# Kernel tuning notes

Measured on AMD Instinct MI355X. Metric: run time of the kernel, lower is better.

Reference implementation:

```python
import jax, jax.numpy as jnp
import numpy as np

K = 3      # kernel size
PAD = 1    # kernel_size // 2


def _deform_conv(x, offset, w_def):
    """mmcv DeformConv (deform_groups=1, stride=1, dilation=1, no bias).
    x: [B,C,H,W], offset: [B,2*K*K,H,W] ordered (dy,dx) per kernel tap, w_def: [O,C,K,K].
    Bilinear sampling with zero padding outside the feature map.
    """
    B, C, H, W = x.shape
    kk = K * K
    off = offset.reshape(B, kk, 2, H, W)
    # kernel-tap grid (row-major: ky, kx)
    ar = jnp.arange(K)
    gy, gx = jnp.meshgrid(ar, ar, indexing='ij')
    gy = gy.reshape(kk)
    gx = gx.reshape(kk)
    hh = jnp.arange(H, dtype=x.dtype)
    ww = jnp.arange(W, dtype=x.dtype)
    # sampling positions: p0 - pad + kernel tap + learned offset  -> [B,kk,H,W]
    ys = hh[None, None, :, None] - PAD + gy[None, :, None, None] + off[:, :, 0]
    xs = ww[None, None, None, :] - PAD + gx[None, :, None, None] + off[:, :, 1]

    y0 = jnp.floor(ys)
    x0 = jnp.floor(xs)
    ly = ys - y0
    lx = xs - x0

    xf = x.reshape(B, C, H * W)

    def gather(yi, xi):
        valid = (yi >= 0) & (yi <= H - 1) & (xi >= 0) & (xi <= W - 1)
        yc = jnp.clip(yi, 0, H - 1).astype(jnp.int32)
        xc = jnp.clip(xi, 0, W - 1).astype(jnp.int32)
        idx = (yc * W + xc).reshape(B, 1, kk * H * W)
        g = jnp.take_along_axis(xf, idx, axis=2).reshape(B, C, kk, H, W)
        return g * valid.reshape(B, 1, kk, H, W).astype(x.dtype)

    # bilinear interpolation, per-corner zero masking == zero padding
    v = (gather(y0, x0) * ((1 - ly) * (1 - lx))[:, None]
         + gather(y0, x0 + 1) * ((1 - ly) * lx)[:, None]
         + gather(y0 + 1, x0) * (ly * (1 - lx))[:, None]
         + gather(y0 + 1, x0 + 1) * (ly * lx)[:, None])  # [B,C,kk,H,W]

    O = w_def.shape[0]
    return jnp.einsum('bckhw,ock->bohw', v, w_def.reshape(O, C, kk))


def setup_inputs() -> dict:
    key = jax.random.key(0)
    k1, k2, k3, k4 = jax.random.split(key, 4)
    B, C_in, C_off, C_out, H, W = 4, 128, 64, 128, 128, 128
    x = jax.random.normal(k1, (B, C_in, H, W), dtype=jnp.float32)
    off = jax.random.normal(k2, (B, C_off, H, W), dtype=jnp.float32)
    # NOTE: the torch module zero-inits the offset conv; we use small random
    # weights so the deformable gather path is actually exercised.
    w_off = 0.1 * jax.random.normal(k3, (2 * K * K, C_off), dtype=jnp.float32)
    b_off = jnp.zeros((2 * K * K,), dtype=jnp.float32)
    w_def = jax.random.normal(k4, (C_out, C_in, K, K), dtype=jnp.float32) / np.sqrt(C_in * K * K)
    return {"x": x, "off": off, "w_off": w_off, "b_off": b_off, "w_def": w_def}


def reference(x, off, w_off, b_off, w_def):
    # 1x1 offset conv
    offset = jnp.einsum('oc,bchw->bohw', w_off, off) + b_off[None, :, None, None]
    # deformable conv + ReLU
    return jax.nn.relu(_deform_conv(x, offset, w_def))
```

## Files before the change

### kernel.cpp

```cpp
#include <hip/hip_runtime.h>
#include <stdint.h>

typedef __attribute__((ext_vector_type(8))) short short8;
typedef __attribute__((ext_vector_type(4))) float f32x4;

constexpr int Hc = 128, Wc = 128, HWc = Hc * Wc;
constexpr int Cin = 128, Cout = 128;
constexpr int OffC = 18, OffIn = 64;

__device__ __forceinline__ float bf2f(unsigned short u) {
    return __builtin_bit_cast(float, (unsigned)u << 16);
}
__device__ __forceinline__ unsigned short f2bf(float f) {
    unsigned u = __builtin_bit_cast(unsigned, f);
    return (unsigned short)((u + 0x7FFFu + ((u >> 16) & 1u)) >> 16);
}

__global__ void k_offconv(const float* __restrict__ off, const float* __restrict__ w_off,
                          const float* __restrict__ b_off, float* __restrict__ offset) {
    __shared__ float wsm[OffC * OffIn];
    __shared__ float bsm[OffC];
    int tid = threadIdx.x;
    for (int i = tid; i < OffC * OffIn; i += 256) wsm[i] = w_off[i];
    if (tid < OffC) bsm[tid] = b_off[tid];
    __syncthreads();
    int g = blockIdx.x * 256 + tid;
    int b = g >> 14, hw = g & (HWc - 1);
    const float* offb = off + b * OffIn * HWc + hw;
    float acc[OffC];
#pragma unroll
    for (int o = 0; o < OffC; ++o) acc[o] = bsm[o];
    for (int c = 0; c < OffIn; ++c) {
        float v = offb[c << 14];
#pragma unroll
        for (int o = 0; o < OffC; ++o) acc[o] += wsm[o * OffIn + c] * v;
    }
    float* outb = offset + b * OffC * HWc + hw;
#pragma unroll
    for (int o = 0; o < OffC; ++o) outb[o << 14] = acc[o];
}

__global__ void k_xpose(const float* __restrict__ x, unsigned short* __restrict__ xt) {
    __shared__ float tile[128][65];
    int blk = blockIdx.x;
    int b = blk >> 8;
    int hw0 = (blk & 255) << 6;
    const float* xb = x + b * Cin * HWc;
    int tid = threadIdx.x;
#pragma unroll
    for (int k = 0; k < 32; ++k) {
        int e = tid + k * 256;
        int c = e >> 6, p = e & 63;
        tile[c][p] = xb[(c << 14) + hw0 + p];
    }
    __syncthreads();
    unsigned short* xtb = xt + ((b << 14) + hw0) * Cin;
#pragma unroll
    for (int k = 0; k < 16; ++k) {
        int e = (tid + k * 256) * 2;
        int p = e >> 7, c = e & 127;
        unsigned lo = f2bf(tile[c][p]);
        unsigned hi = f2bf(tile[c + 1][p]);
        *(unsigned*)(xtb + e) = lo | (hi << 16);
    }
}

__global__ void k_wprep(const float* __restrict__ wd, unsigned short* __restrict__ wt) {
    int i = blockIdx.x * 256 + threadIdx.x;
    int kk = i >> 14, o = (i >> 7) & 127, c = i & 127;
    wt[i] = f2bf(wd[((o << 7) + c) * 9 + kk]);
}

__global__ __launch_bounds__(512, 4)
void k_deform(const unsigned short* __restrict__ xt, const float* __restrict__ offset,
              const unsigned short* __restrict__ wt, float* __restrict__ out) {
    __shared__ float offs[OffC][128];
    __shared__ __align__(16) unsigned short vt[2][128 * 128];

    int tid = threadIdx.x;
    int bid = blockIdx.x;
    int swz = (bid & 7) * 64 + (bid >> 3);
    int b = swz >> 7;
    int hw0 = (swz & 127) << 7;

    const float* offg = offset + b * OffC * HWc + hw0;
    for (int i = tid; i < OffC * 128; i += 512)
        offs[i >> 7][i & 127] = offg[((i >> 7) << 14) + (i & 127)];
    __syncthreads();

    int px = tid >> 2;
    int cq = tid & 3;
    int c0 = cq * 8;
    int h = (hw0 + px) >> 7, w = (hw0 + px) & 127;
    const unsigned short* xb = xt + (size_t)(b << 14) * Cin;
    char* vtb = (char*)vt;

    float cw[4]; int cb[4];
    auto calc_params = [&](int tap) {
        float dy = offs[2 * tap][px], dx = offs[2 * tap + 1][px];
        float ys = (float)(h - 1 + tap / 3) + dy;
        float xs = (float)(w - 1 + tap % 3) + dx;
        float y0f = floorf(ys), x0f = floorf(xs);
        float ly = ys - y0f, lx = xs - x0f;
        int y0 = (int)y0f, x0 = (int)x0f;
#pragma unroll
        for (int cr = 0; cr < 4; ++cr) {
            int yi = y0 + (cr >> 1), xi = x0 + (cr & 1);
            bool valid = (yi >= 0) && (yi < Hc) && (xi >= 0) && (xi < Wc);
            float wy = (cr >> 1) ? ly : 1.0f - ly;
            float wx = (cr & 1) ? lx : 1.0f - lx;
            int yc = yi < 0 ? 0 : (yi > Hc - 1 ? Hc - 1 : yi);
            int xc = xi < 0 ? 0 : (xi > Wc - 1 ? Wc - 1 : xi);
            cw[cr] = valid ? wy * wx : 0.0f;
            cb[cr] = ((yc << 7) + xc) << 7;
        }
    };
    auto issue = [&](short8* r, int i) {
#pragma unroll
        for (int cr = 0; cr < 4; ++cr)
            r[cr] = *(const short8*)(xb + cb[cr] + c0 + i * 32);
    };
    auto consume = [&](short8* r, int i, int buf) {
        float v[8];
#pragma unroll
        for (int k = 0; k < 8; ++k) {
            v[k] = cw[0] * bf2f((unsigned short)r[0][k])
                 + cw[1] * bf2f((unsigned short)r[1][k])
                 + cw[2] * bf2f((unsigned short)r[2][k])
                 + cw[3] * bf2f((unsigned short)r[3][k]);
        }
        short8 pk;
#pragma unroll
        for (int k = 0; k < 8; ++k) pk[k] = (short)f2bf(v[k]);
        int byteoff = ((px << 8) + ((c0 + i * 32) << 1)) ^ ((px & 7) << 4);
        *(short8*)(vtb + buf * 32768 + byteoff) = pk;
    };

    int lane = tid & 63, wave = tid >> 6;
    int obase = (wave >> 2) << 6;
    int pbase = (wave & 3) << 5;

    f32x4 acc[4][2];
#pragma unroll
    for (int i = 0; i < 4; ++i)
#pragma unroll
        for (int j = 0; j < 2; ++j)
            acc[i][j] = (f32x4){0.f, 0.f, 0.f, 0.f};

    auto mfma_half = [&](int buf, int tap, int kb0) {
        const unsigned short* wtap = wt + (tap << 14);
#pragma unroll
        for (int kb = kb0; kb < kb0 + 2; ++kb) {
            int kc = (kb << 5) + ((lane >> 4) << 3);
            int p0 = pbase + (lane & 15);
            int p1 = p0 + 16;
            short8 b0 = *(const short8*)(vtb + buf * 32768 + ((((p0 << 8) + (kc << 1)) ^ ((p0 & 7) << 4))));
            short8 b1 = *(const short8*)(vtb + buf * 32768 + ((((p1 << 8) + (kc << 1)) ^ ((p1 & 7) << 4))));
            short8 aa[4];
#pragma unroll
            for (int ot = 0; ot < 4; ++ot)
                aa[ot] = *(const short8*)(wtap + (obase + (ot << 4) + (lane & 15)) * 128 + kc);
#pragma unroll
            for (int ot = 0; ot < 4; ++ot) {
                acc[ot][0] = __builtin_amdgcn_mfma_f32_16x16x32_bf16(aa[ot], b0, acc[ot][0], 0, 0, 0);
                acc[ot][1] = __builtin_amdgcn_mfma_f32_16x16x32_bf16(aa[ot], b1, acc[ot][1], 0, 0, 0);
            }
        }
    };

    short8 r0[4], r1[4];

    calc_params(0);
    issue(r0, 0); issue(r1, 1);
    consume(r0, 0, 0); issue(r0, 2);
    consume(r1, 1, 0); issue(r1, 3);
    consume(r0, 2, 0); consume(r1, 3, 0);
    __syncthreads();

    for (int t = 0; t < 9; ++t) {
        int cur = t & 1;
        if (t < 8) {
            calc_params(t + 1);
            issue(r0, 0); issue(r1, 1);
        }
        mfma_half(cur, t, 0);
        if (t < 8) {
            consume(r0, 0, cur ^ 1); issue(r0, 2);
            consume(r1, 1, cur ^ 1); issue(r1, 3);
        }
        mfma_half(cur, t, 2);
        if (t < 8) {
            consume(r0, 2, cur ^ 1); consume(r1, 3, cur ^ 1);
        }
        __syncthreads();
    }

    float* outb = out + (size_t)(b * Cout) * HWc + hw0;
#pragma unroll
    for (int ot = 0; ot < 4; ++ot)
#pragma unroll
        for (int pb = 0; pb < 2; ++pb)
#pragma unroll
            for (int j = 0; j < 4; ++j) {
                int o = obase + (ot << 4) + ((lane >> 4) << 2) + j;
                int p = pbase + (pb << 4) + (lane & 15);
                float v = acc[ot][pb][j];
                outb[(o << 14) + p] = v > 0.f ? v : 0.f;
            }
}

extern "C" void kernel_launch(void* const* d_in, const int* in_sizes, int n_in,
                              void* d_out, int out_size, void* d_ws, size_t ws_size,
                              hipStream_t stream) {
    const float* x     = (const float*)d_in[0];
    const float* off   = (const float*)d_in[1];
    const float* w_off = (const float*)d_in[2];
    const float* b_off = (const float*)d_in[3];
    const float* w_def = (const float*)d_in[4];
    float* out = (float*)d_out;

    char* ws = (char*)d_ws;
    float* offset      = (float*)ws;
    unsigned short* xt = (unsigned short*)(ws + 4718592);
    unsigned short* wt = (unsigned short*)(ws + 4718592 + 16777216);

    hipLaunchKernelGGL(k_offconv, dim3(256),  dim3(256), 0, stream, off, w_off, b_off, offset);
    hipLaunchKernelGGL(k_xpose,   dim3(1024), dim3(256), 0, stream, x, xt);
    hipLaunchKernelGGL(k_wprep,   dim3(576),  dim3(256), 0, stream, w_def, wt);
    hipLaunchKernelGGL(k_deform,  dim3(512),  dim3(512), 0, stream, xt, offset, wt, out);
}
```

Measured before the change: 206.7 us.

## Gather bilinear samples directly into MFMA B-fragments, dropping LDS staging

The deform kernel no longer stages the offsets and blended samples in shared memory with double buffering and barriers. Each wave now loads its own offsets, gathers the four bilinear corners straight into the register layout the MFMA B operand expects, and blends them in registers. Each wave now covers all 128 output channels for 32 pixels, with 256-thread blocks instead of 512. This removes LDS traffic and __syncthreads, but each block reads every weight fragment four times from global/L2 and holds more accumulator registers, and gather latency is no longer overlapped with compute.

```diff
diff --git a/kernel.cpp b/kernel.cpp
--- a/kernel.cpp
+++ b/kernel.cpp
@@ -71,33 +71,33 @@
     wt[i] = f2bf(wd[((o << 7) + c) * 9 + kk]);
 }
 
-__global__ __launch_bounds__(512, 4)
+__global__ __launch_bounds__(256)
 void k_deform(const unsigned short* __restrict__ xt, const float* __restrict__ offset,
               const unsigned short* __restrict__ wt, float* __restrict__ out) {
-    __shared__ float offs[OffC][128];
-    __shared__ __align__(16) unsigned short vt[2][128 * 128];
-
     int tid = threadIdx.x;
+    int lane = tid & 63, wave = tid >> 6;
     int bid = blockIdx.x;
     int swz = (bid & 7) * 64 + (bid >> 3);
     int b = swz >> 7;
     int hw0 = (swz & 127) << 7;
+    int p0 = hw0 + (wave << 5) + (lane & 15);
+    int p1 = p0 + 16;
+    int cg = lane >> 4;
 
-    const float* offg = offset + b * OffC * HWc + hw0;
-    for (int i = tid; i < OffC * 128; i += 512)
-        offs[i >> 7][i & 127] = offg[((i >> 7) << 14) + (i & 127)];
-    __syncthreads();
+    const unsigned short* xb = xt + ((size_t)b << 21);
+    const float* offp = offset + (size_t)b * (OffC * HWc);
 
-    int px = tid >> 2;
-    int cq = tid & 3;
-    int c0 = cq * 8;
-    int h = (hw0 + px) >> 7, w = (hw0 + px) & 127;
-    const unsigned short* xb = xt + (size_t)(b << 14) * Cin;
-    char* vtb = (char*)vt;
+    int h0 = p0 >> 7, w0 = p0 & 127;
+    int h1 = p1 >> 7, w1 = p1 & 127;
 
-    float cw[4]; int cb[4];
-    auto calc_params = [&](int tap) {
-        float dy = offs[2 * tap][px], dx = offs[2 * tap + 1][px];
+    f32x4 acc[8][2];
+#pragma unroll
+    for (int i = 0; i < 8; ++i)
+#pragma unroll
+        for (int j = 0; j < 2; ++j)
+            acc[i][j] = (f32x4){0.f, 0.f, 0.f, 0.f};
+
+    auto cparm = [&](int tap, float dy, float dx, int h, int w, float* cw, int* cb) {
         float ys = (float)(h - 1 + tap / 3) + dy;
         float xs = (float)(w - 1 + tap % 3) + dx;
         float y0f = floorf(ys), x0f = floorf(xs);
@@ -115,97 +115,65 @@
             cb[cr] = ((yc << 7) + xc) << 7;
         }
     };
-    auto issue = [&](short8* r, int i) {
-#pragma unroll
-        for (int cr = 0; cr < 4; ++cr)
-            r[cr] = *(const short8*)(xb + cb[cr] + c0 + i * 32);
-    };
-    auto consume = [&](short8* r, int i, int buf) {
-        float v[8];
-#pragma unroll
-        for (int k = 0; k < 8; ++k) {
-            v[k] = cw[0] * bf2f((unsigned short)r[0][k])
-                 + cw[1] * bf2f((unsigned short)r[1][k])
-                 + cw[2] * bf2f((unsigned short)r[2][k])
-                 + cw[3] * bf2f((unsigned short)r[3][k]);
-        }
+
+    auto blend = [&](const short8* r, const float* cw) -> short8 {
         short8 pk;
 #pragma unroll
-        for (int k = 0; k < 8; ++k) pk[k] = (short)f2bf(v[k]);
-        int byteoff = ((px << 8) + ((c0 + i * 32) << 1)) ^ ((px & 7) << 4);
-        *(short8*)(vtb + buf * 32768 + byteoff) = pk;
+        for (int j = 0; j < 8; ++j) {
+            float v = cw[0] * bf2f((unsigned short)r[0][j])
+                    + cw[1] * bf2f((unsigned short)r[1][j])
+                    + cw[2] * bf2f((unsigned short)r[2][j])
+                    + cw[3] * bf2f((unsigned short)r[3][j]);
+            pk[j] = (short)f2bf(v);
+        }
+        return pk;
     };
 
-    int lane = tid & 63, wave = tid >> 6;
-    int obase = (wave >> 2) << 6;
-    int pbase = (wave & 3) << 5;
+    float cw0[4], cw1[4]; int cb0[4], cb1[4];
+    float dy0 = offp[p0], dx0 = offp[(1 << 14) + p0];
+    float dy1 = offp[p1], dx1 = offp[(1 << 14) + p1];
 
-    f32x4 acc[4][2];
+    for (int t = 0; t < 9; ++t) {
+        cparm(t, dy0, dx0, h0, w0, cw0, cb0);
+        cparm(t, dy1, dx1, h1, w1, cw1, cb1);
+        if (t < 8) {
+            dy0 = offp[((2 * t + 2) << 14) + p0]; dx0 = offp[((2 * t + 3) << 14) + p0];
+            dy1 = offp[((2 * t + 2) << 14) + p1]; dx1 = offp[((2 * t + 3) << 14) + p1];
+        }
+        const unsigned short* wtap = wt + (t << 14);
 #pragma unroll
-    for (int i = 0; i < 4; ++i)
+        for (int ks = 0; ks < 4; ++ks) {
+            int kc = (ks << 5) + (cg << 3);
+            short8 r0[4], r1[4];
 #pragma unroll
-        for (int j = 0; j < 2; ++j)
-            acc[i][j] = (f32x4){0.f, 0.f, 0.f, 0.f};
-
-    auto mfma_half = [&](int buf, int tap, int kb0) {
-        const unsigned short* wtap = wt + (tap << 14);
+            for (int cr = 0; cr < 4; ++cr) {
+                r0[cr] = *(const short8*)(xb + cb0[cr] + kc);
+                r1[cr] = *(const short8*)(xb + cb1[cr] + kc);
+            }
+            short8 A[8];
 #pragma unroll
-        for (int kb = kb0; kb < kb0 + 2; ++kb) {
-            int kc = (kb << 5) + ((lane >> 4) << 3);
-            int p0 = pbase + (lane & 15);
-            int p1 = p0 + 16;
-            short8 b0 = *(const short8*)(vtb + buf * 32768 + ((((p0 << 8) + (kc << 1)) ^ ((p0 & 7) << 4))));
-            short8 b1 = *(const short8*)(vtb + buf * 32768 + ((((p1 << 8) + (kc << 1)) ^ ((p1 & 7) << 4))));
-            short8 aa[4];
+            for (int ot = 0; ot < 8; ++ot)
+                A[ot] = *(const short8*)(wtap + ((ot << 4) + (lane & 15)) * 128 + kc);
+            short8 bf0 = blend(r0, cw0);
+            short8 bf1 = blend(r1, cw1);
 #pragma unroll
-            for (int ot = 0; ot < 4; ++ot)
-                aa[ot] = *(const short8*)(wtap + (obase + (ot << 4) + (lane & 15)) * 128 + kc);
-#pragma unroll
-            for (int ot = 0; ot < 4; ++ot) {
-                acc[ot][0] = __builtin_amdgcn_mfma_f32_16x16x32_bf16(aa[ot], b0, acc[ot][0], 0, 0, 0);
-                acc[ot][1] = __builtin_amdgcn_mfma_f32_16x16x32_bf16(aa[ot], b1, acc[ot][1], 0, 0, 0);
+            for (int ot = 0; ot < 8; ++ot) {
+                acc[ot][0] = __builtin_amdgcn_mfma_f32_16x16x32_bf16(A[ot], bf0, acc[ot][0], 0, 0, 0);
+                acc[ot][1] = __builtin_amdgcn_mfma_f32_16x16x32_bf16(A[ot], bf1, acc[ot][1], 0, 0, 0);
             }
         }
-    };
-
-    short8 r0[4], r1[4];
-
-    calc_params(0);
-    issue(r0, 0); issue(r1, 1);
-    consume(r0, 0, 0); issue(r0, 2);
-    consume(r1, 1, 0); issue(r1, 3);
-    consume(r0, 2, 0); consume(r1, 3, 0);
-    __syncthreads();
-
-    for (int t = 0; t < 9; ++t) {
-        int cur = t & 1;
-        if (t < 8) {
-            calc_params(t + 1);
-            issue(r0, 0); issue(r1, 1);
-        }
-        mfma_half(cur, t, 0);
-        if (t < 8) {
-            consume(r0, 0, cur ^ 1); issue(r0, 2);
-            consume(r1, 1, cur ^ 1); issue(r1, 3);
-        }
-        mfma_half(cur, t, 2);
-        if (t < 8) {
-            consume(r0, 2, cur ^ 1); consume(r1, 3, cur ^ 1);
-        }
-        __syncthreads();
     }
 
-    float* outb = out + (size_t)(b * Cout) * HWc + hw0;
 #pragma unroll
-    for (int ot = 0; ot < 4; ++ot)
+    for (int ot = 0; ot < 8; ++ot)
 #pragma unroll
-        for (int pb = 0; pb < 2; ++pb)
+        for (int pt = 0; pt < 2; ++pt)
 #pragma unroll
             for (int j = 0; j < 4; ++j) {
-                int o = obase + (ot << 4) + ((lane >> 4) << 2) + j;
-                int p = pbase + (pb << 4) + (lane & 15);
-                float v = acc[ot][pb][j];
-                outb[(o << 14) + p] = v > 0.f ? v : 0.f;
+                int o = (ot << 4) + ((lane >> 4) << 2) + j;
+                int px = hw0 + (wave << 5) + (pt << 4) + (lane & 15);
+                float v = acc[ot][pt][j];
+                out[(((size_t)(b << 7) + o) << 14) + px] = v > 0.f ? v : 0.f;
             }
 }
 
@@ -227,5 +195,5 @@
     hipLaunchKernelGGL(k_offconv, dim3(256),  dim3(256), 0, stream, off, w_off, b_off, offset);
     hipLaunchKernelGGL(k_xpose,   dim3(1024), dim3(256), 0, stream, x, xt);
     hipLaunchKernelGGL(k_wprep,   dim3(576),  dim3(256), 0, stream, w_def, wt);
-    hipLaunchKernelGGL(k_deform,  dim3(512),  dim3(512), 0, stream, xt, offset, wt, out);
+    hipLaunchKernelGGL(k_deform,  dim3(512),  dim3(256), 0, stream, xt, offset, wt, out);
 }
```

After: 240.6 us. +16.4%, slower.
